# Kernel tuning notes

Hardware: AMD Instinct MI355X
Metric: run time of the kernel (lower is better)

Reference implementation:

```python
import jax, jax.numpy as jnp
import numpy as np

PS = 8          # patch size
D_STATE = 16
D_CONV = 4
DT_RANK = 6     # ceil(96/16)
N_HEADS = 2
NEG = jnp.float32(-1e30)
_DIRS = np.array([[-1, 0], [1, 0], [0, -1], [0, 1]], np.int32)


def _ln(x, w, b, eps=1e-5):
    mu = x.mean(-1, keepdims=True)
    var = ((x - mu) ** 2).mean(-1, keepdims=True)
    return (x - mu) * jax.lax.rsqrt(var + eps) * w + b


def _vit_score_map(x, pos_embed, proj_w, proj_b, in_w, in_b, out_w, out_b,
                   ln1_w, ln1_b, ff1_w, ff1_b, ff2_w, ff2_b, ln2_w, ln2_b,
                   score_w, score_b):
    B, C, H, W = x.shape
    Hp, Wp = H // PS, W // PS
    N = Hp * Wp
    E = proj_w.shape[0]
    # F.unfold ordering: per patch the vector is (C, kr, kc) flattened
    patches = x.reshape(B, C, Hp, PS, Wp, PS).transpose(0, 2, 4, 1, 3, 5).reshape(B, N, C * PS * PS)
    patches = patches @ proj_w.T + proj_b
    if pos_embed.shape[1] != N:
        o = int(pos_embed.shape[1] ** 0.5)
        pe = jax.image.resize(pos_embed.reshape(1, o, o, E), (1, Hp, Wp, E), 'bilinear').reshape(1, N, E)
    else:
        pe = pos_embed
    patches = patches + 0.1 * pe
    # nn.TransformerEncoderLayer defaults: post-norm, ReLU, eval (no dropout)
    qkv = patches @ in_w.T + in_b
    q, k, v = jnp.split(qkv, 3, axis=-1)
    dh = E // N_HEADS
    def heads(t):
        return t.reshape(B, N, N_HEADS, dh).transpose(0, 2, 1, 3)
    q, k, v = heads(q), heads(k), heads(v)
    attn = jax.nn.softmax(jnp.einsum('bhqd,bhkd->bhqk', q, k) / np.float32(np.sqrt(dh)), axis=-1)
    ctx = jnp.einsum('bhqk,bhkd->bhqd', attn, v).transpose(0, 2, 1, 3).reshape(B, N, E)
    src = _ln(patches + (ctx @ out_w.T + out_b), ln1_w, ln1_b)
    ff = jax.nn.relu(src @ ff1_w.T + ff1_b) @ ff2_w.T + ff2_b
    src = _ln(src + ff, ln2_w, ln2_b)
    scores = jax.nn.sigmoid((src @ score_w.T + score_b)[..., 0])
    pvar = patches.var(axis=-1, ddof=1)          # torch.var is unbiased
    final = 0.7 * scores + 0.3 * jax.nn.sigmoid(pvar * 10.0)
    return final.reshape(B, Hp, Wp)


def _traversal(score):
    """Greedy adaptive patch traversal: start at global argmax, walk to the best
    unvisited 4-neighbor; on dead-end jump to the global argmax over unvisited."""
    Hp, Wp = score.shape
    n = Hp * Wp
    s = score.reshape(-1)
    dirs = jnp.asarray(_DIRS)
    start = jnp.argmax(s).astype(jnp.int32)
    visited0 = jnp.zeros((n,), bool).at[start].set(True)

    def step(carry, _):
        visited, cur = carry
        ci, cj = cur // Wp, cur % Wp
        ni, nj = ci + dirs[:, 0], cj + dirs[:, 1]
        valid = (ni >= 0) & (ni < Hp) & (nj >= 0) & (nj < Wp)
        nidx = (jnp.clip(ni, 0, Hp - 1) * Wp + jnp.clip(nj, 0, Wp - 1)).astype(jnp.int32)
        nsc = jnp.where(valid & ~visited[nidx], s[nidx], NEG)
        b = jnp.argmax(nsc)                       # first-max tie-break == '>' loop order
        jump = jnp.argmax(jnp.where(visited, NEG, s)).astype(jnp.int32)
        nxt = jnp.where(nsc[b] > NEG * 0.5, nidx[b], jump).astype(jnp.int32)
        return (visited.at[nxt].set(True), nxt), nxt

    _, rest = jax.lax.scan(step, (visited0, start), None, length=n - 1)
    return jnp.concatenate([start[None], rest])


def _mamba(u, in_w, conv_w, conv_b, xproj_w, dt_w, dt_b, A_log, D_skip, out_w):
    B, L, _ = u.shape
    d_in = conv_w.shape[0]
    xz = u @ in_w.T                               # (B,L,2*d_in)
    xx, z = jnp.split(xz, 2, axis=-1)
    # causal depthwise conv over sequence
    xc = jnp.pad(xx.transpose(0, 2, 1), ((0, 0), (0, 0), (D_CONV - 1, 0)))
    xc = jax.lax.conv_general_dilated(xc, conv_w, (1,), 'VALID',
                                      feature_group_count=d_in,
                                      dimension_numbers=('NCH', 'OIH', 'NCH'))
    xx = jax.nn.silu((xc + conv_b[None, :, None]).transpose(0, 2, 1))   # (B,L,d_in)
    dbl = xx @ xproj_w.T
    dt, Bm, Cm = jnp.split(dbl, [DT_RANK, DT_RANK + D_STATE], axis=-1)
    dt = jax.nn.softplus(dt @ dt_w.T + dt_b)      # (B,L,d_in)
    A = -jnp.exp(A_log)                           # (d_in, d_state)

    def step(h, inp):
        dt_t, B_t, C_t, x_t = inp                 # (B,d_in),(B,ds),(B,ds),(B,d_in)
        h = jnp.exp(dt_t[..., None] * A) * h + (dt_t * x_t)[..., None] * B_t[:, None, :]
        return h, jnp.einsum('bds,bs->bd', h, C_t)

    h0 = jnp.zeros((B, d_in, D_STATE), u.dtype)
    xs = (dt.transpose(1, 0, 2), Bm.transpose(1, 0, 2), Cm.transpose(1, 0, 2), xx.transpose(1, 0, 2))
    _, ys = jax.lax.scan(step, h0, xs)
    y = ys.transpose(1, 0, 2) + xx * D_skip
    return (y * jax.nn.silu(z)) @ out_w.T


def setup_inputs() -> dict:
    key = jax.random.key(0)
    ks = jax.random.split(key, 20)
    B, C, H, W = 2, 96, 128, 128
    E, FF = 96, 2048
    d_in, dr, ds, dc = 192, 6, 16, 4
    f32 = jnp.float32
    def w(k, shape, s=0.02):
        return jax.random.normal(k, shape, f32) * s
    return dict(
        x=jax.random.normal(ks[0], (B, C, H, W), f32),
        pe=w(ks[1], (B, H * W, C), 0.02),
        pos_embed=w(ks[2], (1, 784, E)),
        vit_proj_w=w(ks[3], (E, C * PS * PS)),
        vit_proj_b=jnp.zeros((E,), f32),
        attn_in_w=w(ks[4], (3 * E, E)),
        attn_in_b=jnp.zeros((3 * E,), f32),
        attn_out_w=w(ks[5], (E, E)),
        attn_out_b=jnp.zeros((E,), f32),
        ln1_w=jnp.ones((E,), f32), ln1_b=jnp.zeros((E,), f32),
        ff1_w=w(ks[6], (FF, E)), ff1_b=jnp.zeros((FF,), f32),
        ff2_w=w(ks[7], (E, FF)), ff2_b=jnp.zeros((E,), f32),
        ln2_w=jnp.ones((E,), f32), ln2_b=jnp.zeros((E,), f32),
        score_w=w(ks[8], (1, E)), score_b=jnp.zeros((1,), f32),
        norm_w=jnp.ones((C,), f32), norm_b=jnp.zeros((C,), f32),
        in_proj_w=w(ks[9], (2 * d_in, C)),
        conv_w=w(ks[10], (d_in, 1, dc), 0.1),
        conv_b=jnp.zeros((d_in,), f32),
        x_proj_w=w(ks[11], (dr + 2 * ds, d_in)),
        dt_w=w(ks[12], (d_in, dr)),
        dt_b=jnp.full((d_in,), -4.6, f32),        # softplus(dt_b) ~ 0.01 (mamba dt init)
        A_log=jnp.log(jnp.tile(jnp.arange(1, ds + 1, dtype=f32), (d_in, 1))),
        D_skip=jnp.ones((d_in,), f32),
        out_proj_w=w(ks[13], (C, d_in)),
    )


def reference(x, pe, pos_embed, vit_proj_w, vit_proj_b, attn_in_w, attn_in_b,
              attn_out_w, attn_out_b, ln1_w, ln1_b, ff1_w, ff1_b, ff2_w, ff2_b,
              ln2_w, ln2_b, score_w, score_b, norm_w, norm_b, in_proj_w,
              conv_w, conv_b, x_proj_w, dt_w, dt_b, A_log, D_skip, out_proj_w):
    B, C, H, W = x.shape
    n = H * W
    # Dynamic_Adaptive_Scan with the code's DCNv3Function-is-None fallback:
    # x = input_last, permuted back to channels-first => identity on x.
    x_adapted = x
    score_map = _vit_score_map(x_adapted, pos_embed, vit_proj_w, vit_proj_b,
                               attn_in_w, attn_in_b, attn_out_w, attn_out_b,
                               ln1_w, ln1_b, ff1_w, ff1_b, ff2_w, ff2_b,
                               ln2_w, ln2_b, score_w, score_b)
    order = jax.vmap(_traversal)(jax.lax.stop_gradient(score_map))    # (B, Hp*Wp)
    Hp, Wp = score_map.shape[1], score_map.shape[2]
    pi, pj = order // Wp, order % Wp
    # expand each patch into its PSxPS pixels in raster order
    offs = (jnp.arange(PS, dtype=jnp.int32)[:, None] * W + jnp.arange(PS, dtype=jnp.int32)[None, :]).reshape(-1)
    idx = ((pi * PS * W + pj * PS)[..., None] + offs).reshape(B, n)    # (B, n)
    x_tok = jnp.take_along_axis(x_adapted.reshape(B, C, n), idx[:, None, :], axis=2).transpose(0, 2, 1)
    pe_r = jnp.take_along_axis(pe, idx[..., None], axis=1)
    tokens = _ln(x_tok + pe_r, norm_w, norm_b)
    y = _mamba(tokens, in_proj_w, conv_w, conv_b, x_proj_w, dt_w, dt_b, A_log, D_skip, out_proj_w)
    # scatter back to spatial raster order
    out = jax.vmap(lambda yb, ib: jnp.zeros_like(yb).at[ib].set(yb))(y, idx)
    return out.transpose(0, 2, 1).reshape(B, C, H, W)
```

## Files before the change

### kernel.cpp

```cpp
#include <hip/hip_runtime.h>
#include <math.h>

#define BB 2
#define CC 96
#define HH 128
#define WW 128
#define PS 8
#define HP 16
#define WP 16
#define NPATCH 256
#define EE 96
#define FF 2048
#define DH 48
#define DIN 192
#define DR 6
#define DS 16
#define LL 16384
#define NCHUNK 512
#define CLEN 32
#define NSEG 16
#define SEGC 32
#define KTOT 6144
#define KSPLIT 32
#define KSL 192
// ... 166 lines not shown
  }
  float2 mx = red[0]; __syncthreads();
  float ev0 = expf(sc0 - mx.x), ev1 = expf(sc1 - mx.y);
  red[tid] = make_float2(ev0, ev1); __syncthreads();
  for(int stp=128; stp>0; stp>>=1){
    if(tid<stp){ float2 o=red[tid+stp]; red[tid].x+=o.x; red[tid].y+=o.y; }
    __syncthreads();
  }
  float2 dn = red[0]; __syncthreads();
  p0[tid] = ev0/dn.x; p1[tid] = ev1/dn.y;
  __syncthreads();
  if(tid < 192){
    int dd = tid % EE, jh = tid / EE;
    const float* vb = base + 192 + dd;
    const float* pp = (dd < DH) ? p0 : p1;
    float acc0 = 0.f, acc1 = 0.f;
    #pragma unroll 4
    for(int j=jh*128; j<jh*128+128; j+=2){
      acc0 += pp[j]*vb[(size_t)j*288];
      acc1 += pp[j+1]*vb[(size_t)(j+1)*288];
    }
    part[jh][dd] = acc0+acc1;
  }
  __syncthreads();
  if(tid < EE) ctxs[tid] = part[0][tid] + part[1][tid];
  __syncthreads();
  float o = 0.f;
  if(tid < EE){
    const float4* ar = (const float4*)ctxs;
    const float4* wr = (const float4*)(ow + (size_t)tid*EE);
    float4 s4 = {0.f,0.f,0.f,0.f};
    #pragma unroll
    for(int k=0;k<24;k++){
      float4 av=ar[k], wv=wr[k];
      s4.x += av.x*wv.x; s4.y += av.y*wv.y; s4.z += av.z*wv.z; s4.w += av.w*wv.w;
    }
    o = ob[tid] + (s4.x+s4.y)+(s4.z+s4.w) + patches[(size_t)gb*EE + tid];
  }
  if(tid < 128){
    float sv = o, sq = o*o;
    for(int off=32; off>0; off>>=1){ sv += __shfl_xor(sv, off); sq += __shfl_xor(sq, off); }
    if((tid&63)==0){ ps[tid>>6]=sv; pq2[tid>>6]=sq; }
  }
  __syncthreads();
  if(tid==0){
    float s = ps[0]+ps[1], qq = pq2[0]+pq2[1];
    float mu = s/EE;
    st[0]=mu; st[1]=rsqrtf(qq/EE - mu*mu + 1e-5f);
  }
  __syncthreads();
  if(tid < EE) src1[(size_t)gb*EE + tid] = (o-st[0])*st[1]*lw[tid] + lb[tid];
}

__global__ __launch_bounds__(512) void k_ff1(const float* __restrict__ src1,
    const float* __restrict__ w1, const float* __restrict__ b1, float* __restrict__ ffh){
  int row0 = blockIdx.x*2; int tid = threadIdx.x;
  const float4* a0 = (const float4*)(src1 + (size_t)row0*EE);
  const float4* a1 = (const float4*)(src1 + (size_t)(row0+1)*EE);
  for(int fo=0;fo<4;fo++){
    int f = fo*512 + tid;
    const float4* wr = (const float4*)(w1 + (size_t)f*EE);
    float bc = b1[f];
    float acc0=bc, acc1=bc;
    #pragma unroll
    for(int k=0;k<24;k++){
      float4 wv = wr[k];
      float4 av;
      av = a0[k]; acc0 += av.x*wv.x+av.y*wv.y+av.z*wv.z+av.w*wv.w;
      av = a1[k]; acc1 += av.x*wv.x+av.y*wv.y+av.z*wv.z+av.w*wv.w;
    }
    ffh[(size_t)(row0+0)*FF + f] = fmaxf(acc0, 0.f);
    ffh[(size_t)(row0+1)*FF + f] = fmaxf(acc1, 0.f);
  }
}

__global__ __launch_bounds__(384) void k_ff2_score(const float* __restrict__ ffh,
    const float* __restrict__ w2, const float* __restrict__ b2,
    const float* __restrict__ src1, const float* __restrict__ lw,
    const float* __restrict__ lb, const float* __restrict__ sw,
    const float* __restrict__ sb, const float* __restrict__ pvar,
    float* __restrict__ fscore){
  __shared__ float partl[8][EE];
  __shared__ float s2[2][EE];
  __shared__ float psr[2][2], pqr[2][2], str[2][2];
  int row0 = blockIdx.x*2; int tid = threadIdx.x;
  int e = tid % EE, fg = tid / EE;
  const float4* wr = (const float4*)(w2 + (size_t)e*FF + fg*512);
  const float4* h0 = (const float4*)(ffh + (size_t)row0*FF + fg*512);
  const float4* h1 = (const float4*)(ffh + (size_t)(row0+1)*FF + fg*512);
  float acc0=0.f, acc1=0.f;
  #pragma unroll 4
  for(int k=0;k<128;k++){
    float4 wv = wr[k];
    float4 hv;
    hv = h0[k]; acc0 += hv.x*wv.x+hv.y*wv.y+hv.z*wv.z+hv.w*wv.w;
    hv = h1[k]; acc1 += hv.x*wv.x+hv.y*wv.y+hv.z*wv.z+hv.w*wv.w;
  }
  partl[0*4+fg][e] = acc0;
  partl[1*4+fg][e] = acc1;
  __syncthreads();
  if(tid < 192){
    int r = tid / EE, e2 = tid % EE;
    float s = partl[r*4+0][e2] + partl[r*4+1][e2] + partl[r*4+2][e2] + partl[r*4+3][e2];
    s2[r][e2] = s + b2[e2] + src1[(size_t)(row0+r)*EE + e2];
  }
  __syncthreads();
  int g = tid >> 7, t = tid & 127;
  float v = 0.f;
  if(g < 2){
    v = (t < EE) ? s2[g][t] : 0.f;
    float sv = v, sq = v*v;
    for(int off=32; off>0; off>>=1){ sv += __shfl_xor(sv, off); sq += __shfl_xor(sq, off); }
    if((t&63)==0){ psr[g][t>>6]=sv; pqr[g][t>>6]=sq; }
  }
  __syncthreads();
  if(g < 2 && t == 0){
    float s = psr[g][0]+psr[g][1], qq = pqr[g][0]+pqr[g][1];
    float mu = s/EE;
    str[g][0]=mu; str[g][1]=rsqrtf(qq/EE - mu*mu + 1e-5f);
  }
  __syncthreads();
  if(g < 2){
    float o = (t < EE) ? ((v-str[g][0])*str[g][1]*lw[t] + lb[t]) * sw[t] : 0.f;
    for(int off=32; off>0; off>>=1) o += __shfl_xor(o, off);
    if((t&63)==0) psr[g][t>>6] = o;
  }
  __syncthreads();
  if(g < 2 && t == 0){
    float acc = psr[g][0]+psr[g][1] + sb[0];
    fscore[row0+g] = 0.7f*sigmoid_acc(acc) + 0.3f*sigmoid_acc(pvar[row0+g]*10.f);
  }
}

__global__ __launch_bounds__(768) void k_trav_fused(const float* __restrict__ fscore,
    const float* __restrict__ x, const float* __restrict__ pe,
    const float* __restrict__ nw, const float* __restrict__ nb,
    const float* __restrict__ w, int* __restrict__ pixmap,
    float* __restrict__ xx, float* __restrict__ z){
  __shared__ float fsl[NPATCH];
  __shared__ int   sidxl[NPATCH];
  __shared__ int   ordl[NPATCH];
  __shared__ float a[32*100];
  __shared__ float ps[12*384];
  int tid = threadIdx.x;
  if(blockIdx.x < 2){
    int b = blockIdx.x;
    int lane = tid;
    if(lane < 64){
      for(int k=lane;k<NPATCH;k+=64) fsl[k] = fscore[b*NPATCH+k];
    }
    __syncthreads();
    if(lane < 64){
// ... 68 lines not shown
        float v2 = (lane<32) ? a[t*100 + 64 + lane] : 0.f;
        float sv = v1+v2, sq = v1*v1 + v2*v2;
        for(int off=32; off>0; off>>=1){ sv += __shfl_xor(sv, off); sq += __shfl_xor(sq, off); }
        float mu = sv/EE;
        float rs = rsqrtf(sq/EE - mu*mu + 1e-5f);
        a[t*100 + lane] = (v1-mu)*rs*nw[lane] + nb[lane];
        if(lane < 32) a[t*100 + 64 + lane] = (v2-mu)*rs*nw[64+lane] + nb[64+lane];
      }
    }
    __syncthreads();
    int kh = tid/384, col = tid - kh*384;
    float4 wv[12];
    const float4* wr4 = (const float4*)(w + (size_t)col*EE + kh*48);
    #pragma unroll
    for(int i=0;i<12;i++) wv[i] = wr4[i];
    #pragma unroll
    for(int g=0; g<3; g++){
      float acc[12];
      #pragma unroll
      for(int r=0;r<12;r++){
        int gi = g*12 + r;
        if(gi < 32){
          const float4* ar = (const float4*)(a + gi*100 + kh*48);
          float4 s4 = {0.f,0.f,0.f,0.f};
          #pragma unroll
          for(int i=0;i<12;i++){
            float4 av = ar[i];
            s4.x += av.x*wv[i].x; s4.y += av.y*wv[i].y; s4.z += av.z*wv[i].z; s4.w += av.w*wv[i].w;
          }
          acc[r] = (s4.x+s4.y)+(s4.z+s4.w);
        } else acc[r] = 0.f;
      }
      if(kh==1){
        #pragma unroll
        for(int r=0;r<12;r++) if(g*12+r < 32) ps[r*384 + col] = acc[r];
      }
      __syncthreads();
      if(kh==0){
        #pragma unroll
        for(int r=0;r<12;r++){
          int gi = g*12 + r;
          if(gi < 32){
            float tot = acc[r] + ps[r*384 + col];
            if(col < DIN) xx[(size_t)(R0 + gi)*DIN + col] = tot;
            else          z [(size_t)(R0 + gi)*DIN + (col - DIN)] = tot;
          }
        }
      }
      __syncthreads();
    }
  }
}

__global__ __launch_bounds__(256) void k_convgather(const float* __restrict__ xx,
    const int* __restrict__ pixmap, const float* __restrict__ cw,
    const float* __restrict__ cb, float* __restrict__ xc){
  __shared__ int pixl[35];
  __shared__ float xxl[35*DIN];
  int blk = blockIdx.x; int b = blk>>9; int l0 = (blk&511)*32;
  int tid = threadIdx.x;
  if(tid < 35){
    int l = l0 - 3 + tid;
    pixl[tid] = (l >= 0) ? pixmap[b*LL + l] : 0;
  }
  __syncthreads();
  for(int i=tid; i<35*DIN; i+=256){
    int rr = i/DIN, d = i - rr*DIN;
    int l = l0 - 3 + rr;
    xxl[i] = (l >= 0) ? xx[((size_t)b*LL + pixl[rr])*DIN + d] : 0.f;
  }
  __syncthreads();
  for(int i=tid; i<32*DIN; i+=256){
    int rr = i/DIN, d = i - rr*DIN;
    float v = cb[d]
      + cw[d*4+0]*xxl[(rr+0)*DIN + d]
      + cw[d*4+1]*xxl[(rr+1)*DIN + d]
      + cw[d*4+2]*xxl[(rr+2)*DIN + d]
      + cw[d*4+3]*xxl[(rr+3)*DIN + d];
    xc[((size_t)b*LL + l0 + rr)*DIN + d] = v * sigmoid_fast(v);
  }
}

__global__ __launch_bounds__(320) void k_xproj(const float* __restrict__ xc, const float* __restrict__ xpw,
    const float* __restrict__ dtw, const float* __restrict__ dtb,
    float* __restrict__ dt, float* __restrict__ Bm, float* __restrict__ Cm){
  __shared__ float a[8][196];
  __shared__ float dbl[8][40];
  int rb = blockIdx.x; size_t row0 = (size_t)rb*8;
  int tid = threadIdx.x;
  for(int i=tid;i<8*DIN;i+=320){ int r=i/DIN, k=i%DIN; a[r][k] = xc[(row0+r)*DIN + k]; }
  __syncthreads();
  {
    int r = tid & 7, o = tid >> 3;
    if(o < 38){
      const float4* wr = (const float4*)(xpw + (size_t)o*DIN);
      const float4* ar = (const float4*)(a[r]);
      float4 s4 = {0.f,0.f,0.f,0.f};
      #pragma unroll
      for(int k=0;k<48;k++){
        float4 av=ar[k], wv=wr[k];
        s4.x += av.x*wv.x; s4.y += av.y*wv.y; s4.z += av.z*wv.z; s4.w += av.w*wv.w;
      }
      dbl[r][o] = (s4.x+s4.y)+(s4.z+s4.w);
    }
  }
  __syncthreads();
  for(int t=tid;t<8*DIN;t+=320){
    int r = t/DIN, d = t%DIN;
    float acc = dtb[d];
    #pragma unroll
    for(int j=0;j<DR;j++) acc += dbl[r][j]*dtw[d*DR+j];
    dt[(row0+r)*DIN + d] = fmaxf(acc, 0.f) + log1pf(__expf(-fabsf(acc)));
  }
  if(tid < 8*DS){
    int r = tid/DS, s = tid%DS;
    Bm[(row0+r)*DS + s] = dbl[r][6+s];
    Cm[(row0+r)*DS + s] = dbl[r][22+s];
  }
}

__global__ __launch_bounds__(192) void k_scan1(const float* __restrict__ dt,
    const float* __restrict__ xc, const float* __restrict__ Bm,
    const float* __restrict__ Alog, float* __restrict__ hend, float* __restrict__ sumdt){
  int blk = blockIdx.x;
  int b = blk >> 9, c = blk & (NCHUNK-1);
  int d = threadIdx.x;
  float A[16];
  {
    const float4* a4 = (const float4*)(Alog + d*DS);
    #pragma unroll
    for(int i=0;i<4;i++){
      float4 v = a4[i];
      A[i*4+0]=-expf(v.x); A[i*4+1]=-expf(v.y); A[i*4+2]=-expf(v.z); A[i*4+3]=-expf(v.w);
    }
  }
  float h[16];
  #pragma unroll
  for(int s=0;s<16;s++) h[s]=0.f;
  float sd = 0.f;
  size_t base = (size_t)b*LL + (size_t)c*CLEN;
  const float* dp = dt + base*DIN + d;
  const float* xp = xc + base*DIN + d;
  const float4* bp = (const float4*)(Bm + base*DS);
  for(int t=0;t<CLEN;t++){
    float dtv = dp[(size_t)t*DIN];
    float xv  = xp[(size_t)t*DIN];
    float4 b0=bp[t*4+0], b1=bp[t*4+1], b2=bp[t*4+2], b3=bp[t*4+3];
    float e[16];
    #pragma unroll
    for(int s=0;s<16;s++) e[s] = __expf(dtv*A[s]);
    float Bv[16] = {b0.x,b0.y,b0.z,b0.w,b1.x,b1.y,b1.z,b1.w,b2.x,b2.y,b2.z,b2.w,b3.x,b3.y,b3.z,b3.w};
    float dx = dtv*xv; sd += dtv;
    #pragma unroll
    for(int s=0;s<16;s++) h[s] = e[s]*h[s] + dx*Bv[s];
  }
  size_t o = ((size_t)c*BB + b)*DIN + d;
  float4* hp = (float4*)(hend + o*DS);
  hp[0] = make_float4(h[0],h[1],h[2],h[3]);
  hp[1] = make_float4(h[4],h[5],h[6],h[7]);
  hp[2] = make_float4(h[8],h[9],h[10],h[11]);
  hp[3] = make_float4(h[12],h[13],h[14],h[15]);
  sumdt[o] = sd;
}

__global__ __launch_bounds__(256) void k_scan2a(const float* __restrict__ hend,
    const float* __restrict__ sumdt, const float* __restrict__ Alog,
    float* __restrict__ segP, float* __restrict__ segH){
  int g = blockIdx.x*256 + threadIdx.x;
  int seg = g / 6144; int r = g % 6144;
  int b = r / 3072; int d = (r % 3072) >> 4; int s = r & 15;
  float A = -expf(Alog[d*DS + s]);
  float P = 1.f, H = 0.f;
  int c0 = seg*SEGC;
  for(int cc=0; cc<SEGC; cc+=4){
    float sd[4], he[4];
    #pragma unroll
    for(int j=0;j<4;j++){
      size_t o = ((size_t)(c0+cc+j)*BB + b)*DIN + d;
      sd[j] = sumdt[o]; he[j] = hend[o*DS + s];
    }
    #pragma unroll
    for(int j=0;j<4;j++){
      float aa = __expf(A*sd[j]);
      H = aa*H + he[j]; P *= aa;
    }
  }
  segP[seg*6144 + r] = P; segH[seg*6144 + r] = H;
}

__global__ void k_scan2b(const float* __restrict__ segP, const float* __restrict__ segH,
                         float* __restrict__ segHin){
  int r = blockIdx.x*256 + threadIdx.x;
  float P[NSEG], H[NSEG];
  #pragma unroll
  for(int sg=0; sg<NSEG; sg++){ P[sg]=segP[sg*6144+r]; H[sg]=segH[sg*6144+r]; }
  float h = 0.f;
  #pragma unroll
  for(int sg=0; sg<NSEG; sg++){
    segHin[sg*6144 + r] = h;
    h = P[sg]*h + H[sg];
  }
}

__global__ __launch_bounds__(256) void k_scan2c(float* __restrict__ hend,
    const float* __restrict__ sumdt, const float* __restrict__ Alog,
    const float* __restrict__ segHin){
  int g = blockIdx.x*256 + threadIdx.x;
  int seg = g / 6144; int r = g % 6144;
  int b = r / 3072; int d = (r % 3072) >> 4; int s = r & 15;
  float A = -expf(Alog[d*DS + s]);
  float h = segHin[seg*6144 + r];
  int c0 = seg*SEGC;
  for(int cc=0; cc<SEGC; cc+=4){
    float sd[4], he[4]; size_t oo[4];
    #pragma unroll
    for(int j=0;j<4;j++){
      oo[j] = ((size_t)(c0+cc+j)*BB + b)*DIN + d;
      sd[j] = sumdt[oo[j]]; he[j] = hend[oo[j]*DS + s];
    }
    #pragma unroll
    for(int j=0;j<4;j++){
      hend[oo[j]*DS + s] = h;
      float aa = __expf(A*sd[j]);
      h = aa*h + he[j];
    }
  }
}

__global__ __launch_bounds__(192) void k_scan3(const float* __restrict__ dt,
    const float* __restrict__ xc, const float* __restrict__ Bm, const float* __restrict__ Cm,
    const float* __restrict__ Alog, const float* __restrict__ hin,
    const float* __restrict__ Dskip, const int* __restrict__ pixmap,
    float* __restrict__ z){
  __shared__ int pixs[CLEN];
  int blk = blockIdx.x;
  int b = blk >> 9, c = blk & (NCHUNK-1);
  int d = threadIdx.x;
  if(d < CLEN) pixs[d] = pixmap[b*LL + c*CLEN + d];
  float A[16];
  {
    const float4* a4 = (const float4*)(Alog + d*DS);
    #pragma unroll
    for(int i=0;i<4;i++){
      float4 v = a4[i];
      A[i*4+0]=-expf(v.x); A[i*4+1]=-expf(v.y); A[i*4+2]=-expf(v.z); A[i*4+3]=-expf(v.w);
    }
  }
  size_t o = ((size_t)c*BB + b)*DIN + d;
  float h[16];
  {
    const float4* hi = (const float4*)(hin + o*DS);
    #pragma unroll
    for(int i=0;i<4;i++){
      float4 v = hi[i];
      h[i*4+0]=v.x; h[i*4+1]=v.y; h[i*4+2]=v.z; h[i*4+3]=v.w;
    }
  }
  float Dv = Dskip[d];
  size_t base = (size_t)b*LL + (size_t)c*CLEN;
  const float* dp = dt + base*DIN + d;
  const float* xp = xc + base*DIN + d;
  const float4* bp = (const float4*)(Bm + base*DS);
  const float4* cp = (const float4*)(Cm + base*DS);
  __syncthreads();
  for(int t=0;t<CLEN;t++){
    float dtv = dp[(size_t)t*DIN];
    float xv  = xp[(size_t)t*DIN];
    size_t zrow = ((size_t)b*LL + pixs[t])*DIN + d;
    float zv  = z[zrow];
    float4 b0=bp[t*4+0], b1=bp[t*4+1], b2=bp[t*4+2], b3=bp[t*4+3];
    float4 c0=cp[t*4+0], c1=cp[t*4+1], c2=cp[t*4+2], c3=cp[t*4+3];
    float e[16];
    #pragma unroll
    for(int s=0;s<16;s++) e[s] = __expf(dtv*A[s]);
    float Bv[16] = {b0.x,b0.y,b0.z,b0.w,b1.x,b1.y,b1.z,b1.w,b2.x,b2.y,b2.z,b2.w,b3.x,b3.y,b3.z,b3.w};
    float Cv[16] = {c0.x,c0.y,c0.z,c0.w,c1.x,c1.y,c1.z,c1.w,c2.x,c2.y,c2.z,c2.w,c3.x,c3.y,c3.z,c3.w};
    float dx = dtv*xv;
    float y = 0.f;
    #pragma unroll
    for(int s=0;s<16;s++){ h[s] = e[s]*h[s] + dx*Bv[s]; y += h[s]*Cv[s]; }
    float yy = y + xv*Dv;
    z[zrow] = yy * (zv * sigmoid_fast(zv));
  }
}

__global__ __launch_bounds__(384) void k_outproj(const float* __restrict__ g,
    const float* __restrict__ w, float* __restrict__ ytok){
  __shared__ float a[16*DIN];
  __shared__ float psA[16*EE];
  __shared__ float psB[16*EE];
  int rb = blockIdx.x; size_t row0 = (size_t)rb*16;
  int tid = threadIdx.x;
  int col = tid % EE, kq = tid / EE;
  {
    const float4* src = (const float4*)(g + row0*DIN);
    float4* ad = (float4*)a;
    ad[tid] = src[tid];
    ad[tid+384] = src[tid+384];
  }
  float4 wv[12];
  const float4* wr4 = (const float4*)(w + (size_t)col*DIN + kq*48);
  #pragma unroll
  for(int i=0;i<12;i++) wv[i] = wr4[i];
  __syncthreads();
  float acc[16];
  for(int r=0;r<16;r++){
    const float4* ar = (const float4*)(a + r*DIN + kq*48);
    float4 s4 = {0.f,0.f,0.f,0.f};
    #pragma unroll
    for(int i=0;i<12;i++){
      float4 av = ar[i];
      s4.x += av.x*wv[i].x; s4.y += av.y*wv[i].y; s4.z += av.z*wv[i].z; s4.w += av.w*wv[i].w;
    }
    acc[r] = (s4.x+s4.y)+(s4.z+s4.w);
  }
  if(kq==1){
    for(int r=0;r<16;r++) psA[r*EE+col] = acc[r];
  }
  if(kq==3){
    for(int r=0;r<16;r++) psB[r*EE+col] = acc[r];
  }
  __syncthreads();
  if(kq==0){
    for(int r=0;r<16;r++) acc[r] += psA[r*EE+col];
  }
  if(kq==2){
    for(int r=0;r<16;r++) acc[r] += psB[r*EE+col];
  }
  __syncthreads();
  if(kq==2){
    for(int r=0;r<16;r++) psA[r*EE+col] = acc[r];
  }
  __syncthreads();
  if(kq==0){
    for(int r=0;r<16;r++) ytok[(row0+r)*EE + col] = acc[r] + psA[r*EE+col];
  }
}

__global__ __launch_bounds__(256) void k_scatter(const float* __restrict__ ytok,
    float* __restrict__ out){
  __shared__ float yt[64*100];
  int gb = blockIdx.x; int b = gb>>8, ch = gb&255;
  int tid = threadIdx.x;
  for(int i=tid;i<64*24;i+=256){
    int q = i/24, c4 = i%24;
    float4 v = ((const float4*)(ytok + ((size_t)b*LL + ch*64 + q)*EE))[c4];
    ((float4*)(yt + q*100))[c4] = v;
  }
  __syncthreads();
  int q = tid&63; int cg = tid>>6;
  int pix = ch*64 + q;
  for(int c=cg;c<CC;c+=4){
    out[(((size_t)(b*CC + c))<<14) + pix] = yt[q*100 + c];
  }
}

extern "C" void kernel_launch(void* const* d_in, const int* in_sizes, int n_in,
                              void* d_out, int out_size, void* d_ws, size_t ws_size,
                              hipStream_t stream){
  (void)in_sizes; (void)n_in; (void)out_size; (void)ws_size;
  const float* x    = (const float*)d_in[0];
  const float* pe   = (const float*)d_in[1];
  const float* pos  = (const float*)d_in[2];
  const float* vw   = (const float*)d_in[3];
  const float* vb   = (const float*)d_in[4];
  const float* inw  = (const float*)d_in[5];
  const float* inb  = (const float*)d_in[6];
  const float* ow   = (const float*)d_in[7];
  const float* ob   = (const float*)d_in[8];
  const float* l1w  = (const float*)d_in[9];
  const float* l1b  = (const float*)d_in[10];
  const float* f1w  = (const float*)d_in[11];
  const float* f1b  = (const float*)d_in[12];
  const float* f2w  = (const float*)d_in[13];
  const float* f2b  = (const float*)d_in[14];
  const float* l2w  = (const float*)d_in[15];
  const float* l2b  = (const float*)d_in[16];
  const float* sw   = (const float*)d_in[17];
  const float* sb   = (const float*)d_in[18];
  const float* nw   = (const float*)d_in[19];
  const float* nb   = (const float*)d_in[20];
  const float* ipw  = (const float*)d_in[21];
  const float* cw   = (const float*)d_in[22];
  const float* cb   = (const float*)d_in[23];
  const float* xpw  = (const float*)d_in[24];
  const float* dtw  = (const float*)d_in[25];
  const float* dtbp = (const float*)d_in[26];
  const float* alog = (const float*)d_in[27];
  const float* dsk  = (const float*)d_in[28];
  const float* opw  = (const float*)d_in[29];
  float* out = (float*)d_out;

  char* wsb = (char*)d_ws;
  size_t off = 0;
  auto alloc = [&](size_t nfloats)->void*{
    void* p = (void*)(wsb + off);
    off += ((nfloats*sizeof(float) + 255) & ~(size_t)255);
    return p;
  };
  float* pe16    = (float*)alloc(256*96);
  float* patches = (float*)alloc(512*96);
  float* pvar    = (float*)alloc(512);
  float* qkv     = (float*)alloc((size_t)512*288);
  float* src1    = (float*)alloc(512*96);
  float* ffh     = (float*)alloc((size_t)512*2048);
  float* fscore  = (float*)alloc(512);
  int*   pixmap  = (int*)  alloc((size_t)2*16384);
  float* tokens  = (float*)alloc((size_t)2*16384*96);
  float* xxb     = (float*)alloc((size_t)2*16384*192);
  float* zb      = (float*)alloc((size_t)2*16384*192);
  float* xcb     = (float*)alloc((size_t)2*16384*192);
  float* Bmat    = (float*)alloc((size_t)2*16384*16);
  float* Cmat    = (float*)alloc((size_t)2*16384*16);
  float* sumdt   = (float*)alloc((size_t)NCHUNK*2*192);
  float* segP    = (float*)alloc((size_t)NSEG*6144);
  float* segH    = (float*)alloc((size_t)NSEG*6144);
  float* segHin  = (float*)alloc((size_t)NSEG*6144);
  float* dtbuf = xxb;
  float* Wt    = xxb;
  float* part  = tokens;
  float* hend  = tokens;
  float* hin   = hend;
  float* ytok  = tokens;

  k_resize_pe   <<<256,   96, 0, stream>>>(pos, pe16);
  k_wtr         <<<96,   256, 0, stream>>>(vw, Wt);
  k_pproj       <<<1024, 384, 0, stream>>>(x, Wt, part);
  k_preduce_qkv <<<512,  320, 0, stream>>>(part, vb, pe16, inw, inb, patches, pvar, qkv);
  k_attn_ln1    <<<512,  256, 0, stream>>>(qkv, ow, ob, patches, l1w, l1b, src1);
  k_ff1         <<<256,  512, 0, stream>>>(src1, f1w, f1b, ffh);
  k_ff2_score   <<<256,  384, 0, stream>>>(ffh, f2w, f2b, src1, l2w, l2b, sw, sb, pvar, fscore);
  k_trav_fused  <<<1026, 768, 0, stream>>>(fscore, x, pe, nw, nb, ipw, pixmap, xxb, zb);
  k_convgather  <<<1024, 256, 0, stream>>>(xxb, pixmap, cw, cb, xcb);
  k_xproj       <<<4096, 320, 0, stream>>>(xcb, xpw, dtw, dtbp, dtbuf, Bmat, Cmat);
  k_scan1       <<<1024, 192, 0, stream>>>(dtbuf, xcb, Bmat, alog, hend, sumdt);
  k_scan2a      <<<384,  256, 0, stream>>>(hend, sumdt, alog, segP, segH);
  k_scan2b      <<<24,   256, 0, stream>>>(segP, segH, segHin);
  k_scan2c      <<<384,  256, 0, stream>>>(hend, sumdt, alog, segHin);
  k_scan3       <<<1024, 192, 0, stream>>>(dtbuf, xcb, Bmat, Cmat, alog, hin, dsk, pixmap, zb);
  k_outproj     <<<2048, 384, 0, stream>>>(zb, opw, ytok);
  k_scatter     <<<512,  256, 0, stream>>>(ytok, out);
}
```

Baseline: 448.7 us.

## Fuse FFN kernels, fuse conv+xproj+scan1, recompute dt in scan3, fold scatter into outproj

Merges ff1 and ff2_score into one kernel that keeps the 2048-wide hidden activations in shared memory, so the ffh buffer never goes to global memory. Fuses conv/gather, x-projection, softplus dt and the chunk-local scan into one per-chunk kernel that works from shared memory. It writes only xc and a compact 40-wide dt-rank/B/C buffer, and scan3 recomputes dt from that buffer instead of reading a 192-wide dt array. Outproj writes straight into the channel-major output with float4 stores, which removes the separate scatter kernel and the ytok round trip. The cost is larger shared-memory use per block (lower occupancy) and duplicated softplus work in scan3.

```diff
diff --git a/kernel.cpp b/kernel.cpp
--- a/kernel.cpp
+++ b/kernel.cpp
@@ -242,52 +242,53 @@
   if(tid < EE) src1[(size_t)gb*EE + tid] = (o-st[0])*st[1]*lw[tid] + lb[tid];
 }
 
-__global__ __launch_bounds__(512) void k_ff1(const float* __restrict__ src1,
-    const float* __restrict__ w1, const float* __restrict__ b1, float* __restrict__ ffh){
-  int row0 = blockIdx.x*2; int tid = threadIdx.x;
-  const float4* a0 = (const float4*)(src1 + (size_t)row0*EE);
-  const float4* a1 = (const float4*)(src1 + (size_t)(row0+1)*EE);
-  for(int fo=0;fo<4;fo++){
-    int f = fo*512 + tid;
-    const float4* wr = (const float4*)(w1 + (size_t)f*EE);
-    float bc = b1[f];
-    float acc0=bc, acc1=bc;
-    #pragma unroll
-    for(int k=0;k<24;k++){
-      float4 wv = wr[k];
-      float4 av;
-      av = a0[k]; acc0 += av.x*wv.x+av.y*wv.y+av.z*wv.z+av.w*wv.w;
-      av = a1[k]; acc1 += av.x*wv.x+av.y*wv.y+av.z*wv.z+av.w*wv.w;
-    }
-    ffh[(size_t)(row0+0)*FF + f] = fmaxf(acc0, 0.f);
-    ffh[(size_t)(row0+1)*FF + f] = fmaxf(acc1, 0.f);
-  }
-}
-
-__global__ __launch_bounds__(384) void k_ff2_score(const float* __restrict__ ffh,
+__global__ __launch_bounds__(512) void k_ffn(const float* __restrict__ src1,
+    const float* __restrict__ w1, const float* __restrict__ b1,
     const float* __restrict__ w2, const float* __restrict__ b2,
-    const float* __restrict__ src1, const float* __restrict__ lw,
-    const float* __restrict__ lb, const float* __restrict__ sw,
-    const float* __restrict__ sb, const float* __restrict__ pvar,
-    float* __restrict__ fscore){
+    const float* __restrict__ lw, const float* __restrict__ lb,
+    const float* __restrict__ sw, const float* __restrict__ sb,
+    const float* __restrict__ pvar, float* __restrict__ fscore){
+  __shared__ float hr[2][FF];
   __shared__ float partl[8][EE];
   __shared__ float s2[2][EE];
   __shared__ float psr[2][2], pqr[2][2], str[2][2];
   int row0 = blockIdx.x*2; int tid = threadIdx.x;
-  int e = tid % EE, fg = tid / EE;
-  const float4* wr = (const float4*)(w2 + (size_t)e*FF + fg*512);
-  const float4* h0 = (const float4*)(ffh + (size_t)row0*FF + fg*512);
-  const float4* h1 = (const float4*)(ffh + (size_t)(row0+1)*FF + fg*512);
-  float acc0=0.f, acc1=0.f;
-  #pragma unroll 4
-  for(int k=0;k<128;k++){
-    float4 wv = wr[k];
-    float4 hv;
-    hv = h0[k]; acc0 += hv.x*wv.x+hv.y*wv.y+hv.z*wv.z+hv.w*wv.w;
-    hv = h1[k]; acc1 += hv.x*wv.x+hv.y*wv.y+hv.z*wv.z+hv.w*wv.w;
-  }
-  partl[0*4+fg][e] = acc0;
-  partl[1*4+fg][e] = acc1;
+  {
+    const float4* a0 = (const float4*)(src1 + (size_t)row0*EE);
+    const float4* a1 = (const float4*)(src1 + (size_t)(row0+1)*EE);
+    for(int fo=0;fo<4;fo++){
+      int f = fo*512 + tid;
+      const float4* wr = (const float4*)(w1 + (size_t)f*EE);
+      float bc = b1[f];
+      float acc0=bc, acc1=bc;
+      #pragma unroll
+      for(int k=0;k<24;k++){
+        float4 wv = wr[k];
+        float4 av;
+        av = a0[k]; acc0 += av.x*wv.x+av.y*wv.y+av.z*wv.z+av.w*wv.w;
+        av = a1[k]; acc1 += av.x*wv.x+av.y*wv.y+av.z*wv.z+av.w*wv.w;
+      }
+      hr[0][f] = fmaxf(acc0, 0.f);
+      hr[1][f] = fmaxf(acc1, 0.f);
+    }
+  }
+  __syncthreads();
+  if(tid < 384){
+    int e = tid % EE, fg = tid / EE;
+    const float4* wr = (const float4*)(w2 + (size_t)e*FF + fg*512);
+    const float4* h0 = (const float4*)(hr[0] + fg*512);
+    const float4* h1 = (const float4*)(hr[1] + fg*512);
+    float acc0=0.f, acc1=0.f;
+    #pragma unroll 4
+    for(int k=0;k<128;k++){
+      float4 wv = wr[k];
+      float4 hv;
+      hv = h0[k]; acc0 += hv.x*wv.x+hv.y*wv.y+hv.z*wv.z+hv.w*wv.w;
+      hv = h1[k]; acc1 += hv.x*wv.x+hv.y*wv.y+hv.z*wv.z+hv.w*wv.w;
+    }
+    partl[0*4+fg][e] = acc0;
+    partl[1*4+fg][e] = acc1;
+  }
   __syncthreads();
   if(tid < 192){
     int r = tid / EE, e2 = tid % EE;
@@ -462,12 +463,17 @@
   }
 }
 
-__global__ __launch_bounds__(256) void k_convgather(const float* __restrict__ xx,
-    const int* __restrict__ pixmap, const float* __restrict__ cw,
-    const float* __restrict__ cb, float* __restrict__ xc){
+__global__ __launch_bounds__(256) void k_mamba1(const float* __restrict__ xx,
+    const int* __restrict__ pixmap, const float* __restrict__ cw, const float* __restrict__ cb,
+    const float* __restrict__ xpw, const float* __restrict__ dtw, const float* __restrict__ dtb,
+    const float* __restrict__ Alog, float* __restrict__ xc, float* __restrict__ dblg,
+    float* __restrict__ hend, float* __restrict__ sumdt){
   __shared__ int pixl[35];
   __shared__ float xxl[35*DIN];
-  int blk = blockIdx.x; int b = blk>>9; int l0 = (blk&511)*32;
+  __shared__ float xcl[32*196];
+  __shared__ float dbl[32*40];
+  int blk = blockIdx.x; int b = blk>>9; int c = blk&511;
+  int l0 = c*CLEN;
   int tid = threadIdx.x;
   if(tid < 35){
     int l = l0 - 3 + tid;
@@ -487,90 +493,72 @@
       + cw[d*4+1]*xxl[(rr+1)*DIN + d]
       + cw[d*4+2]*xxl[(rr+2)*DIN + d]
       + cw[d*4+3]*xxl[(rr+3)*DIN + d];
-    xc[((size_t)b*LL + l0 + rr)*DIN + d] = v * sigmoid_fast(v);
-  }
-}
-
-__global__ __launch_bounds__(320) void k_xproj(const float* __restrict__ xc, const float* __restrict__ xpw,
-    const float* __restrict__ dtw, const float* __restrict__ dtb,
-    float* __restrict__ dt, float* __restrict__ Bm, float* __restrict__ Cm){
-  __shared__ float a[8][196];
-  __shared__ float dbl[8][40];
-  int rb = blockIdx.x; size_t row0 = (size_t)rb*8;
-  int tid = threadIdx.x;
-  for(int i=tid;i<8*DIN;i+=320){ int r=i/DIN, k=i%DIN; a[r][k] = xc[(row0+r)*DIN + k]; }
-  __syncthreads();
-  {
-    int r = tid & 7, o = tid >> 3;
-    if(o < 38){
-      const float4* wr = (const float4*)(xpw + (size_t)o*DIN);
-      const float4* ar = (const float4*)(a[r]);
-      float4 s4 = {0.f,0.f,0.f,0.f};
+    float sv = v * sigmoid_fast(v);
+    xcl[rr*196 + d] = sv;
+    xc[((size_t)b*LL + l0 + rr)*DIN + d] = sv;
+  }
+  __syncthreads();
+  for(int task=tid; task<32*38; task+=256){
+    int r = task & 31, o = task >> 5;
+    const float4* wr = (const float4*)(xpw + (size_t)o*DIN);
+    const float4* ar = (const float4*)(xcl + r*196);
+    float4 s4 = {0.f,0.f,0.f,0.f};
+    #pragma unroll
+    for(int k=0;k<48;k++){
+      float4 av=ar[k], wv=wr[k];
+      s4.x += av.x*wv.x; s4.y += av.y*wv.y; s4.z += av.z*wv.z; s4.w += av.w*wv.w;
+    }
+    float val = (s4.x+s4.y)+(s4.z+s4.w);
+    int om = (o<6) ? o : o+2;
+    dbl[r*40 + om] = val;
+    dblg[((size_t)b*LL + l0 + r)*40 + om] = val;
+  }
+  __syncthreads();
+  float* dtl = xxl;
+  for(int i=tid; i<32*DIN; i+=256){
+    int rr = i/DIN, d = i - rr*DIN;
+    float acc = dtb[d];
+    #pragma unroll
+    for(int j=0;j<DR;j++) acc += dbl[rr*40+j]*dtw[d*DR+j];
+    dtl[rr*DIN + d] = fmaxf(acc, 0.f) + log1pf(__expf(-fabsf(acc)));
+  }
+  __syncthreads();
+  if(tid < DIN){
+    int d = tid;
+    float A[16];
+    {
+      const float4* a4 = (const float4*)(Alog + d*DS);
       #pragma unroll
-      for(int k=0;k<48;k++){
-        float4 av=ar[k], wv=wr[k];
-        s4.x += av.x*wv.x; s4.y += av.y*wv.y; s4.z += av.z*wv.z; s4.w += av.w*wv.w;
+      for(int i=0;i<4;i++){
+        float4 v = a4[i];
+        A[i*4+0]=-expf(v.x); A[i*4+1]=-expf(v.y); A[i*4+2]=-expf(v.z); A[i*4+3]=-expf(v.w);
       }
-      dbl[r][o] = (s4.x+s4.y)+(s4.z+s4.w);
-    }
-  }
-  __syncthreads();
-  for(int t=tid;t<8*DIN;t+=320){
-    int r = t/DIN, d = t%DIN;
-    float acc = dtb[d];
-    #pragma unroll
-    for(int j=0;j<DR;j++) acc += dbl[r][j]*dtw[d*DR+j];
-    dt[(row0+r)*DIN + d] = fmaxf(acc, 0.f) + log1pf(__expf(-fabsf(acc)));
-  }
-  if(tid < 8*DS){
-    int r = tid/DS, s = tid%DS;
-    Bm[(row0+r)*DS + s] = dbl[r][6+s];
-    Cm[(row0+r)*DS + s] = dbl[r][22+s];
-  }
-}
-
-__global__ __launch_bounds__(192) void k_scan1(const float* __restrict__ dt,
-    const float* __restrict__ xc, const float* __restrict__ Bm,
-    const float* __restrict__ Alog, float* __restrict__ hend, float* __restrict__ sumdt){
-  int blk = blockIdx.x;
-  int b = blk >> 9, c = blk & (NCHUNK-1);
-  int d = threadIdx.x;
-  float A[16];
-  {
-    const float4* a4 = (const float4*)(Alog + d*DS);
-    #pragma unroll
-    for(int i=0;i<4;i++){
-      float4 v = a4[i];
-      A[i*4+0]=-expf(v.x); A[i*4+1]=-expf(v.y); A[i*4+2]=-expf(v.z); A[i*4+3]=-expf(v.w);
-    }
-  }
-  float h[16];
-  #pragma unroll
-  for(int s=0;s<16;s++) h[s]=0.f;
-  float sd = 0.f;
-  size_t base = (size_t)b*LL + (size_t)c*CLEN;
-  const float* dp = dt + base*DIN + d;
-  const float* xp = xc + base*DIN + d;
-  const float4* bp = (const float4*)(Bm + base*DS);
-  for(int t=0;t<CLEN;t++){
-    float dtv = dp[(size_t)t*DIN];
-    float xv  = xp[(size_t)t*DIN];
-    float4 b0=bp[t*4+0], b1=bp[t*4+1], b2=bp[t*4+2], b3=bp[t*4+3];
-    float e[16];
-    #pragma unroll
-    for(int s=0;s<16;s++) e[s] = __expf(dtv*A[s]);
-    float Bv[16] = {b0.x,b0.y,b0.z,b0.w,b1.x,b1.y,b1.z,b1.w,b2.x,b2.y,b2.z,b2.w,b3.x,b3.y,b3.z,b3.w};
-    float dx = dtv*xv; sd += dtv;
-    #pragma unroll
-    for(int s=0;s<16;s++) h[s] = e[s]*h[s] + dx*Bv[s];
-  }
-  size_t o = ((size_t)c*BB + b)*DIN + d;
-  float4* hp = (float4*)(hend + o*DS);
-  hp[0] = make_float4(h[0],h[1],h[2],h[3]);
-  hp[1] = make_float4(h[4],h[5],h[6],h[7]);
-  hp[2] = make_float4(h[8],h[9],h[10],h[11]);
-  hp[3] = make_float4(h[12],h[13],h[14],h[15]);
-  sumdt[o] = sd;
+    }
+    float h[16];
+    #pragma unroll
+    for(int s=0;s<16;s++) h[s]=0.f;
+    float sd = 0.f;
+    for(int t=0;t<CLEN;t++){
+      float dtv = dtl[t*DIN + d];
+      float xv  = xcl[t*196 + d];
+      const float4* bp4 = (const float4*)(dbl + t*40 + 8);
+      float4 b0=bp4[0], b1=bp4[1], b2=bp4[2], b3=bp4[3];
+      float e[16];
+      #pragma unroll
+      for(int s=0;s<16;s++) e[s] = __expf(dtv*A[s]);
+      float Bv[16] = {b0.x,b0.y,b0.z,b0.w,b1.x,b1.y,b1.z,b1.w,b2.x,b2.y,b2.z,b2.w,b3.x,b3.y,b3.z,b3.w};
+      float dx = dtv*xv; sd += dtv;
+      #pragma unroll
+      for(int s=0;s<16;s++) h[s] = e[s]*h[s] + dx*Bv[s];
+    }
+    size_t o = ((size_t)c*BB + b)*DIN + d;
+    float4* hp = (float4*)(hend + o*DS);
+    hp[0] = make_float4(h[0],h[1],h[2],h[3]);
+    hp[1] = make_float4(h[4],h[5],h[6],h[7]);
+    hp[2] = make_float4(h[8],h[9],h[10],h[11]);
+    hp[3] = make_float4(h[12],h[13],h[14],h[15]);
+    sumdt[o] = sd;
+  }
 }
 
 __global__ __launch_bounds__(256) void k_scan2a(const float* __restrict__ hend,
@@ -637,15 +625,17 @@
   }
 }
 
-__global__ __launch_bounds__(192) void k_scan3(const float* __restrict__ dt,
-    const float* __restrict__ xc, const float* __restrict__ Bm, const float* __restrict__ Cm,
+__global__ __launch_bounds__(192) void k_scan3(const float* __restrict__ xc,
+    const float* __restrict__ dblg, const float* __restrict__ dtw, const float* __restrict__ dtb,
     const float* __restrict__ Alog, const float* __restrict__ hin,
     const float* __restrict__ Dskip, const int* __restrict__ pixmap,
     float* __restrict__ z){
+  __shared__ float dbll[32*40];
   __shared__ int pixs[CLEN];
   int blk = blockIdx.x;
-  int b = blk >> 9, c = blk & (NCHUNK-1);
+  int b = blk >> 9, c = blk & 511;
   int d = threadIdx.x;
+  for(int i=d; i<32*40; i+=192) dbll[i] = dblg[((size_t)b*LL + c*CLEN)*40 + i];
   if(d < CLEN) pixs[d] = pixmap[b*LL + c*CLEN + d];
   float A[16];
   {
@@ -666,20 +656,25 @@
       h[i*4+0]=v.x; h[i*4+1]=v.y; h[i*4+2]=v.z; h[i*4+3]=v.w;
     }
   }
+  float dtwr[DR];
+  #pragma unroll
+  for(int j=0;j<DR;j++) dtwr[j] = dtw[d*DR+j];
+  float dtbd = dtb[d];
   float Dv = Dskip[d];
-  size_t base = (size_t)b*LL + (size_t)c*CLEN;
-  const float* dp = dt + base*DIN + d;
-  const float* xp = xc + base*DIN + d;
-  const float4* bp = (const float4*)(Bm + base*DS);
-  const float4* cp = (const float4*)(Cm + base*DS);
+  const float* xp = xc + ((size_t)b*LL + (size_t)c*CLEN)*DIN + d;
   __syncthreads();
   for(int t=0;t<CLEN;t++){
-    float dtv = dp[(size_t)t*DIN];
+    float acc = dtbd;
+    #pragma unroll
+    for(int j=0;j<DR;j++) acc += dbll[t*40+j]*dtwr[j];
+    float dtv = fmaxf(acc, 0.f) + log1pf(__expf(-fabsf(acc)));
     float xv  = xp[(size_t)t*DIN];
     size_t zrow = ((size_t)b*LL + pixs[t])*DIN + d;
     float zv  = z[zrow];
-    float4 b0=bp[t*4+0], b1=bp[t*4+1], b2=bp[t*4+2], b3=bp[t*4+3];
-    float4 c0=cp[t*4+0], c1=cp[t*4+1], c2=cp[t*4+2], c3=cp[t*4+3];
+    const float4* bp4 = (const float4*)(dbll + t*40 + 8);
+    const float4* cp4 = (const float4*)(dbll + t*40 + 24);
+    float4 b0=bp4[0], b1=bp4[1], b2=bp4[2], b3=bp4[3];
+    float4 c0=cp4[0], c1=cp4[1], c2=cp4[2], c3=cp4[3];
     float e[16];
     #pragma unroll
     for(int s=0;s<16;s++) e[s] = __expf(dtv*A[s]);
@@ -695,11 +690,13 @@
 }
 
 __global__ __launch_bounds__(384) void k_outproj(const float* __restrict__ g,
-    const float* __restrict__ w, float* __restrict__ ytok){
+    const float* __restrict__ w, float* __restrict__ out){
   __shared__ float a[16*DIN];
   __shared__ float psA[16*EE];
   __shared__ float psB[16*EE];
   int rb = blockIdx.x; size_t row0 = (size_t)rb*16;
+  int b = (int)(row0 >> 14);
+  int pix0 = (int)(row0 & 16383);
   int tid = threadIdx.x;
   int col = tid % EE, kq = tid / EE;
   {
@@ -743,25 +740,11 @@
   }
   __syncthreads();
   if(kq==0){
-    for(int r=0;r<16;r++) ytok[(row0+r)*EE + col] = acc[r] + psA[r*EE+col];
-  }
-}
-
-__global__ __launch_bounds__(256) void k_scatter(const float* __restrict__ ytok,
-    float* __restrict__ out){
-  __shared__ float yt[64*100];
-  int gb = blockIdx.x; int b = gb>>8, ch = gb&255;
-  int tid = threadIdx.x;
-  for(int i=tid;i<64*24;i+=256){
-    int q = i/24, c4 = i%24;
-    float4 v = ((const float4*)(ytok + ((size_t)b*LL + ch*64 + q)*EE))[c4];
-    ((float4*)(yt + q*100))[c4] = v;
-  }
-  __syncthreads();
-  int q = tid&63; int cg = tid>>6;
-  int pix = ch*64 + q;
-  for(int c=cg;c<CC;c+=4){
-    out[(((size_t)(b*CC + c))<<14) + pix] = yt[q*100 + c];
+    float4* ob4 = (float4*)(out + (((size_t)(b*CC + col))<<14) + pix0);
+    ob4[0] = make_float4(acc[0]+psA[0*EE+col],  acc[1]+psA[1*EE+col],  acc[2]+psA[2*EE+col],  acc[3]+psA[3*EE+col]);
+    ob4[1] = make_float4(acc[4]+psA[4*EE+col],  acc[5]+psA[5*EE+col],  acc[6]+psA[6*EE+col],  acc[7]+psA[7*EE+col]);
+    ob4[2] = make_float4(acc[8]+psA[8*EE+col],  acc[9]+psA[9*EE+col],  acc[10]+psA[10*EE+col], acc[11]+psA[11*EE+col]);
+    ob4[3] = make_float4(acc[12]+psA[12*EE+col], acc[13]+psA[13*EE+col], acc[14]+psA[14*EE+col], acc[15]+psA[15*EE+col]);
   }
 }
 
@@ -813,41 +796,33 @@
   float* pvar    = (float*)alloc(512);
   float* qkv     = (float*)alloc((size_t)512*288);
   float* src1    = (float*)alloc(512*96);
-  float* ffh     = (float*)alloc((size_t)512*2048);
   float* fscore  = (float*)alloc(512);
   int*   pixmap  = (int*)  alloc((size_t)2*16384);
   float* tokens  = (float*)alloc((size_t)2*16384*96);
   float* xxb     = (float*)alloc((size_t)2*16384*192);
   float* zb      = (float*)alloc((size_t)2*16384*192);
   float* xcb     = (float*)alloc((size_t)2*16384*192);
-  float* Bmat    = (float*)alloc((size_t)2*16384*16);
-  float* Cmat    = (float*)alloc((size_t)2*16384*16);
+  float* dblg    = (float*)alloc((size_t)2*16384*40);
   float* sumdt   = (float*)alloc((size_t)NCHUNK*2*192);
   float* segP    = (float*)alloc((size_t)NSEG*6144);
   float* segH    = (float*)alloc((size_t)NSEG*6144);
   float* segHin  = (float*)alloc((size_t)NSEG*6144);
-  float* dtbuf = xxb;
   float* Wt    = xxb;
   float* part  = tokens;
   float* hend  = tokens;
   float* hin   = hend;
-  float* ytok  = tokens;
 
   k_resize_pe   <<<256,   96, 0, stream>>>(pos, pe16);
   k_wtr         <<<96,   256, 0, stream>>>(vw, Wt);
   k_pproj       <<<1024, 384, 0, stream>>>(x, Wt, part);
   k_preduce_qkv <<<512,  320, 0, stream>>>(part, vb, pe16, inw, inb, patches, pvar, qkv);
   k_attn_ln1    <<<512,  256, 0, stream>>>(qkv, ow, ob, patches, l1w, l1b, src1);
-  k_ff1         <<<256,  512, 0, stream>>>(src1, f1w, f1b, ffh);
-  k_ff2_score   <<<256,  384, 0, stream>>>(ffh, f2w, f2b, src1, l2w, l2b, sw, sb, pvar, fscore);
+  k_ffn         <<<256,  512, 0, stream>>>(src1, f1w, f1b, f2w, f2b, l2w, l2b, sw, sb, pvar, fscore);
   k_trav_fused  <<<1026, 768, 0, stream>>>(fscore, x, pe, nw, nb, ipw, pixmap, xxb, zb);
-  k_convgather  <<<1024, 256, 0, stream>>>(xxb, pixmap, cw, cb, xcb);
-  k_xproj       <<<4096, 320, 0, stream>>>(xcb, xpw, dtw, dtbp, dtbuf, Bmat, Cmat);
-  k_scan1       <<<1024, 192, 0, stream>>>(dtbuf, xcb, Bmat, alog, hend, sumdt);
+  k_mamba1      <<<1024, 256, 0, stream>>>(xxb, pixmap, cw, cb, xpw, dtw, dtbp, alog, xcb, dblg, hend, sumdt);
   k_scan2a      <<<384,  256, 0, stream>>>(hend, sumdt, alog, segP, segH);
   k_scan2b      <<<24,   256, 0, stream>>>(segP, segH, segHin);
   k_scan2c      <<<384,  256, 0, stream>>>(hend, sumdt, alog, segHin);
-  k_scan3       <<<1024, 192, 0, stream>>>(dtbuf, xcb, Bmat, Cmat, alog, hin, dsk, pixmap, zb);
-  k_outproj     <<<2048, 384, 0, stream>>>(zb, opw, ytok);
-  k_scatter     <<<512,  256, 0, stream>>>(ytok, out);
-}
+  k_scan3       <<<1024, 192, 0, stream>>>(xcb, dblg, dtw, dtbp, alog, hin, dsk, pixmap, zb);
+  k_outproj     <<<2048, 384, 0, stream>>>(zb, opw, out);
+}
```

Measured after the change: 461.6 us. 2.9% more time.

## Fuse FFN layers via shared memory and fold scatter into out-projection

Applied to the files above, without the earlier changes.

Merges the two feed-forward kernels into one, keeping the 2048-wide ReLU hidden rows in LDS instead of round-tripping them through a global buffer. It also removes the separate scatter kernel: the output projection now writes straight into the channel-major output with float4 stores over 16 consecutive pixels. This drops two launches and the global traffic for the hidden activations and token outputs. In exchange, the fused FFN block uses 16KB more LDS and leaves 128 threads idle during the second GEMM, and the output writes become strided across channels.

```diff
diff --git a/kernel.cpp b/kernel.cpp
--- a/kernel.cpp
+++ b/kernel.cpp
@@ -242,52 +242,53 @@
   if(tid < EE) src1[(size_t)gb*EE + tid] = (o-st[0])*st[1]*lw[tid] + lb[tid];
 }
 
-__global__ __launch_bounds__(512) void k_ff1(const float* __restrict__ src1,
-    const float* __restrict__ w1, const float* __restrict__ b1, float* __restrict__ ffh){
-  int row0 = blockIdx.x*2; int tid = threadIdx.x;
-  const float4* a0 = (const float4*)(src1 + (size_t)row0*EE);
-  const float4* a1 = (const float4*)(src1 + (size_t)(row0+1)*EE);
-  for(int fo=0;fo<4;fo++){
-    int f = fo*512 + tid;
-    const float4* wr = (const float4*)(w1 + (size_t)f*EE);
-    float bc = b1[f];
-    float acc0=bc, acc1=bc;
-    #pragma unroll
-    for(int k=0;k<24;k++){
-      float4 wv = wr[k];
-      float4 av;
-      av = a0[k]; acc0 += av.x*wv.x+av.y*wv.y+av.z*wv.z+av.w*wv.w;
-      av = a1[k]; acc1 += av.x*wv.x+av.y*wv.y+av.z*wv.z+av.w*wv.w;
-    }
-    ffh[(size_t)(row0+0)*FF + f] = fmaxf(acc0, 0.f);
-    ffh[(size_t)(row0+1)*FF + f] = fmaxf(acc1, 0.f);
-  }
-}
-
-__global__ __launch_bounds__(384) void k_ff2_score(const float* __restrict__ ffh,
+__global__ __launch_bounds__(512) void k_ffn(const float* __restrict__ src1,
+    const float* __restrict__ w1, const float* __restrict__ b1,
     const float* __restrict__ w2, const float* __restrict__ b2,
-    const float* __restrict__ src1, const float* __restrict__ lw,
-    const float* __restrict__ lb, const float* __restrict__ sw,
-    const float* __restrict__ sb, const float* __restrict__ pvar,
-    float* __restrict__ fscore){
+    const float* __restrict__ lw, const float* __restrict__ lb,
+    const float* __restrict__ sw, const float* __restrict__ sb,
+    const float* __restrict__ pvar, float* __restrict__ fscore){
+  __shared__ float hr[2][FF];
   __shared__ float partl[8][EE];
   __shared__ float s2[2][EE];
   __shared__ float psr[2][2], pqr[2][2], str[2][2];
   int row0 = blockIdx.x*2; int tid = threadIdx.x;
-  int e = tid % EE, fg = tid / EE;
-  const float4* wr = (const float4*)(w2 + (size_t)e*FF + fg*512);
-  const float4* h0 = (const float4*)(ffh + (size_t)row0*FF + fg*512);
-  const float4* h1 = (const float4*)(ffh + (size_t)(row0+1)*FF + fg*512);
-  float acc0=0.f, acc1=0.f;
-  #pragma unroll 4
-  for(int k=0;k<128;k++){
-    float4 wv = wr[k];
-    float4 hv;
-    hv = h0[k]; acc0 += hv.x*wv.x+hv.y*wv.y+hv.z*wv.z+hv.w*wv.w;
-    hv = h1[k]; acc1 += hv.x*wv.x+hv.y*wv.y+hv.z*wv.z+hv.w*wv.w;
-  }
-  partl[0*4+fg][e] = acc0;
-  partl[1*4+fg][e] = acc1;
+  {
+    const float4* a0 = (const float4*)(src1 + (size_t)row0*EE);
+    const float4* a1 = (const float4*)(src1 + (size_t)(row0+1)*EE);
+    for(int fo=0;fo<4;fo++){
+      int f = fo*512 + tid;
+      const float4* wr = (const float4*)(w1 + (size_t)f*EE);
+      float bc = b1[f];
+      float acc0=bc, acc1=bc;
+      #pragma unroll
+      for(int k=0;k<24;k++){
+        float4 wv = wr[k];
+        float4 av;
+        av = a0[k]; acc0 += av.x*wv.x+av.y*wv.y+av.z*wv.z+av.w*wv.w;
+        av = a1[k]; acc1 += av.x*wv.x+av.y*wv.y+av.z*wv.z+av.w*wv.w;
+      }
+      hr[0][f] = fmaxf(acc0, 0.f);
+      hr[1][f] = fmaxf(acc1, 0.f);
+    }
+  }
+  __syncthreads();
+  if(tid < 384){
+    int e = tid % EE, fg = tid / EE;
+    const float4* wr = (const float4*)(w2 + (size_t)e*FF + fg*512);
+    const float4* h0 = (const float4*)(hr[0] + fg*512);
+    const float4* h1 = (const float4*)(hr[1] + fg*512);
+    float acc0=0.f, acc1=0.f;
+    #pragma unroll 4
+    for(int k=0;k<128;k++){
+      float4 wv = wr[k];
+      float4 hv;
+      hv = h0[k]; acc0 += hv.x*wv.x+hv.y*wv.y+hv.z*wv.z+hv.w*wv.w;
+      hv = h1[k]; acc1 += hv.x*wv.x+hv.y*wv.y+hv.z*wv.z+hv.w*wv.w;
+    }
+    partl[0*4+fg][e] = acc0;
+    partl[1*4+fg][e] = acc1;
+  }
   __syncthreads();
   if(tid < 192){
     int r = tid / EE, e2 = tid % EE;
@@ -695,11 +696,13 @@
 }
 
 __global__ __launch_bounds__(384) void k_outproj(const float* __restrict__ g,
-    const float* __restrict__ w, float* __restrict__ ytok){
+    const float* __restrict__ w, float* __restrict__ out){
   __shared__ float a[16*DIN];
   __shared__ float psA[16*EE];
   __shared__ float psB[16*EE];
   int rb = blockIdx.x; size_t row0 = (size_t)rb*16;
+  int b = (int)(row0 >> 14);
+  int pix0 = (int)(row0 & 16383);
   int tid = threadIdx.x;
   int col = tid % EE, kq = tid / EE;
   {
@@ -743,25 +746,11 @@
   }
   __syncthreads();
   if(kq==0){
-    for(int r=0;r<16;r++) ytok[(row0+r)*EE + col] = acc[r] + psA[r*EE+col];
-  }
-}
-
-__global__ __launch_bounds__(256) void k_scatter(const float* __restrict__ ytok,
-    float* __restrict__ out){
-  __shared__ float yt[64*100];
-  int gb = blockIdx.x; int b = gb>>8, ch = gb&255;
-  int tid = threadIdx.x;
-  for(int i=tid;i<64*24;i+=256){
-    int q = i/24, c4 = i%24;
-    float4 v = ((const float4*)(ytok + ((size_t)b*LL + ch*64 + q)*EE))[c4];
-    ((float4*)(yt + q*100))[c4] = v;
-  }
-  __syncthreads();
-  int q = tid&63; int cg = tid>>6;
-  int pix = ch*64 + q;
-  for(int c=cg;c<CC;c+=4){
-    out[(((size_t)(b*CC + c))<<14) + pix] = yt[q*100 + c];
+    float4* ob4 = (float4*)(out + (((size_t)(b*CC + col))<<14) + pix0);
+    ob4[0] = make_float4(acc[0]+psA[0*EE+col],  acc[1]+psA[1*EE+col],  acc[2]+psA[2*EE+col],  acc[3]+psA[3*EE+col]);
+    ob4[1] = make_float4(acc[4]+psA[4*EE+col],  acc[5]+psA[5*EE+col],  acc[6]+psA[6*EE+col],  acc[7]+psA[7*EE+col]);
+    ob4[2] = make_float4(acc[8]+psA[8*EE+col],  acc[9]+psA[9*EE+col],  acc[10]+psA[10*EE+col], acc[11]+psA[11*EE+col]);
+    ob4[3] = make_float4(acc[12]+psA[12*EE+col], acc[13]+psA[13*EE+col], acc[14]+psA[14*EE+col], acc[15]+psA[15*EE+col]);
   }
 }
 
@@ -813,7 +802,6 @@
   float* pvar    = (float*)alloc(512);
   float* qkv     = (float*)alloc((size_t)512*288);
   float* src1    = (float*)alloc(512*96);
-  float* ffh     = (float*)alloc((size_t)512*2048);
   float* fscore  = (float*)alloc(512);
   int*   pixmap  = (int*)  alloc((size_t)2*16384);
   float* tokens  = (float*)alloc((size_t)2*16384*96);
@@ -831,15 +819,13 @@
   float* part  = tokens;
   float* hend  = tokens;
   float* hin   = hend;
-  float* ytok  = tokens;
 
   k_resize_pe   <<<256,   96, 0, stream>>>(pos, pe16);
   k_wtr         <<<96,   256, 0, stream>>>(vw, Wt);
   k_pproj       <<<1024, 384, 0, stream>>>(x, Wt, part);
   k_preduce_qkv <<<512,  320, 0, stream>>>(part, vb, pe16, inw, inb, patches, pvar, qkv);
   k_attn_ln1    <<<512,  256, 0, stream>>>(qkv, ow, ob, patches, l1w, l1b, src1);
-  k_ff1         <<<256,  512, 0, stream>>>(src1, f1w, f1b, ffh);
-  k_ff2_score   <<<256,  384, 0, stream>>>(ffh, f2w, f2b, src1, l2w, l2b, sw, sb, pvar, fscore);
+  k_ffn         <<<256,  512, 0, stream>>>(src1, f1w, f1b, f2w, f2b, l2w, l2b, sw, sb, pvar, fscore);
   k_trav_fused  <<<1026, 768, 0, stream>>>(fscore, x, pe, nw, nb, ipw, pixmap, xxb, zb);
   k_convgather  <<<1024, 256, 0, stream>>>(xxb, pixmap, cw, cb, xcb);
   k_xproj       <<<4096, 320, 0, stream>>>(xcb, xpw, dtw, dtbp, dtbuf, Bmat, Cmat);
@@ -848,6 +834,5 @@
   k_scan2b      <<<24,   256, 0, stream>>>(segP, segH, segHin);
   k_scan2c      <<<384,  256, 0, stream>>>(hend, sumdt, alog, segHin);
   k_scan3       <<<1024, 192, 0, stream>>>(dtbuf, xcb, Bmat, Cmat, alog, hin, dsk, pixmap, zb);
-  k_outproj     <<<2048, 384, 0, stream>>>(zb, opw, ytok);
-  k_scatter     <<<512,  256, 0, stream>>>(ytok, out);
-}
+  k_outproj     <<<2048, 384, 0, stream>>>(zb, opw, out);
+}
```

Result: faster. 431.2 us, median of 2 (-3.9%).
